# Optimization experiments

Hardware: AMD Instinct MI355X
Metric: run time of the kernel (lower is better)

Reference implementation:

```python
import jax, jax.numpy as jnp
import numpy as np

B, S, H, NH = 4, 2048, 1024, 16
HD = H // NH
SCALE = 1.0 / np.sqrt(HD)
MASK_VAL = -1e9  # fp32 branch of the torch code


def setup_inputs() -> dict:
    key = jax.random.key(0)
    ks = jax.random.split(key, 6)
    s = 1.0 / np.sqrt(H)
    return {
        "x": jax.random.normal(ks[0], (B, S, H), dtype=jnp.float32),
        "attention_mask": jnp.ones((B, S), dtype=jnp.int32),
        "Wq": jax.random.normal(ks[1], (H, H), dtype=jnp.float32) * s,
        "Wk": jax.random.normal(ks[2], (H, H), dtype=jnp.float32) * s,
        "Wv": jax.random.normal(ks[3], (H, H), dtype=jnp.float32) * s,
        "Wo": jax.random.normal(ks[4], (H, H), dtype=jnp.float32) * s,
        "bo": jnp.zeros((H,), dtype=jnp.float32),
    }


def reference(x, attention_mask, Wq, Wk, Wv, Wo, bo):
    b, s, h = x.shape
    # projections; torch Linear computes x @ W.T
    q = (x @ Wq.T).reshape(b, s, NH, HD).transpose(0, 2, 1, 3)  # [b,nh,s,hd]
    k = (x @ Wk.T).reshape(b, s, NH, HD).transpose(0, 2, 1, 3)
    v = (x @ Wv.T).reshape(b, s, NH, HD).transpose(0, 2, 1, 3)

    scores = jnp.einsum("bhqd,bhkd->bhqk", q, k) * SCALE  # [b,nh,s,s]
    # padding mask: [b,1,1,s]
    pad = (attention_mask == 0)[:, None, None, :]
    scores = jnp.where(pad, MASK_VAL, scores)
    # causal mask
    causal = jnp.tril(jnp.ones((s, s), dtype=bool))[None, None]
    scores = jnp.where(causal, scores, MASK_VAL)

    attn = jax.nn.softmax(scores, axis=-1)  # dropout p=0 / eval -> identity
    out = jnp.einsum("bhqk,bhkd->bhqd", attn, v)
    out = out.transpose(0, 2, 1, 3).reshape(b, s, h)
    return out @ Wo.T + bo
```

## Files before the change

### kernel.cpp

```cpp
#include <hip/hip_runtime.h>

#define B_ 4
#define S_ 2048
#define H_ 1024
#define NH_ 16
#define HD_ 64
#define QSCALE_ 0.1803368801111204f

typedef __attribute__((ext_vector_type(8))) short bf16x8;
typedef __attribute__((ext_vector_type(4))) float f32x4;
typedef __attribute__((ext_vector_type(16))) float f32x16;

__device__ __forceinline__ unsigned short f2bf(float f) {
    unsigned u = __float_as_uint(f);
    unsigned r = (u + 0x7FFFu + ((u >> 16) & 1u)) >> 16;
    return (unsigned short)r;
}
__device__ __forceinline__ float exp2f_hw(float x) { return __builtin_amdgcn_exp2f(x); }

__global__ __launch_bounds__(256) void cast_all(const float* __restrict__ x,
                                                const float* __restrict__ Wq,
                                                const float* __restrict__ Wk,
                                                const float* __restrict__ Wv,
                                                const float* __restrict__ Wo,
                                                unsigned short* __restrict__ xb,
                                                unsigned short* __restrict__ Wqb,
                                                unsigned short* __restrict__ Wkb,
                                                unsigned short* __restrict__ Wvb,
                                                unsigned short* __restrict__ Wob) {
    int bid = blockIdx.x;
    const float* src;
    unsigned short* dst;
    int i;
    if (bid < 8192) {
        src = x; dst = xb; i = bid * 256 + threadIdx.x;
    } else {
        int k = bid - 8192, wsel = k >> 10;
        src = wsel == 0 ? Wq : wsel == 1 ? Wk : wsel == 2 ? Wv : Wo;
        dst = wsel == 0 ? Wqb : wsel == 1 ? Wkb : wsel == 2 ? Wvb : Wob;
        i = (k & 1023) * 256 + threadIdx.x;
    }
    float4 v = reinterpret_cast<const float4*>(src)[i];
    ushort4 o;
    o.x = f2bf(v.x); o.y = f2bf(v.y); o.z = f2bf(v.z); o.w = f2bf(v.w);
    reinterpret_cast<ushort4*>(dst)[i] = o;
}

__device__ __forceinline__ void stage128_swz(const char* g, int gstride, char* lds, int tid) {
    int wave = tid >> 6, lane = tid & 63;
#pragma unroll
    for (int j = 0; j < 4; ++j) {
        int o = ((wave * 4 + j) * 64 + lane) * 16;
        int r = o >> 7;
        int slot = (o >> 4) & 7;
        const char* src = g + (size_t)r * gstride + ((slot ^ (r & 7)) << 4);
        __builtin_amdgcn_global_load_lds((const __attribute__((address_space(1))) void*)src,
                                         (__attribute__((address_space(3))) void*)(lds + (wave * 4 + j) * 1024),
                                         16, 0, 0);
    }
}
__device__ __forceinline__ void stage64_swz8(const char* g, int gstride, char* lds, int tid) {
    int wave = tid >> 6, lane = tid & 63;
    int o = (wave * 64 + lane) * 16;
    int r = o >> 7;
    int slot = (o >> 4) & 7;
    const char* src = g + (size_t)r * gstride + ((slot ^ (r & 7)) << 4);
    __builtin_amdgcn_global_load_lds((const __attribute__((address_space(1))) void*)src,
                                     (__attribute__((address_space(3))) void*)(lds + wave * 1024 + lane * 16),
                                     16, 0, 0);
}

__device__ __forceinline__ bf16x8 frag_swz(const char* lds, int row, int slot) {
    return *reinterpret_cast<const bf16x8*>(lds + row * 128 + (((slot) ^ (row & 7)) << 4));
}

__device__ __forceinline__ float vmax16(const f32x16& v) {
    float a0 = fmaxf(v[0], v[1]), a1 = fmaxf(v[2], v[3]);
    float a2 = fmaxf(v[4], v[5]), a3 = fmaxf(v[6], v[7]);
    float a4 = fmaxf(v[8], v[9]), a5 = fmaxf(v[10], v[11]);
    float a6 = fmaxf(v[12], v[13]), a7 = fmaxf(v[14], v[15]);
    float b0 = fmaxf(a0, a1), b1 = fmaxf(a2, a3), b2 = fmaxf(a4, a5), b3 = fmaxf(a6, a7);
    return fmaxf(fmaxf(b0, b1), fmaxf(b2, b3));
}

__global__ __launch_bounds__(256) void gemm_qkv(const unsigned short* __restrict__ xb,
                                                const unsigned short* __restrict__ Wq,
                                                const unsigned short* __restrict__ Wk,
                                                const unsigned short* __restrict__ Wv,
                                                unsigned short* __restrict__ Qo,
                                                unsigned short* __restrict__ Ko,
                                                unsigned short* __restrict__ Vo) {
    __shared__ __align__(16) char As[2][16384];
    __shared__ __align__(16) char Bs[2][16384];
    int tid = threadIdx.x, lane = tid & 63, wave = tid >> 6;
    int wr = wave >> 1, wc = wave & 1;
    int brow = blockIdx.x * 128;
    int mat = blockIdx.y >> 3;
    int bcol = (blockIdx.y & 7) * 128;
    const unsigned short* W = mat == 0 ? Wq : (mat == 1 ? Wk : Wv);
    unsigned short* O = mat == 0 ? Qo : (mat == 1 ? Ko : Vo);
    float oscale = (mat == 0) ? QSCALE_ : 1.0f;
    f32x4 acc[4][4] = {};
    const char* ga = (const char*)(xb + (size_t)brow * H_);
    const char* gb = (const char*)(W + (size_t)bcol * H_);
    int ro = lane & 15, kg = lane >> 4;
    stage128_swz(ga, H_ * 2, As[0], tid);
    stage128_swz(gb, H_ * 2, Bs[0], tid);
    __syncthreads();
    for (int kt = 0; kt < 16; ++kt) {
        if (kt < 15) {
            stage128_swz(ga + (kt + 1) * 128, H_ * 2, As[(kt + 1) & 1], tid);
            stage128_swz(gb + (kt + 1) * 128, H_ * 2, Bs[(kt + 1) & 1], tid);
        }
        const char* Ac = As[kt & 1];
        const char* Bc = Bs[kt & 1];
#pragma unroll
        for (int kk = 0; kk < 2; ++kk) {
            bf16x8 af[4], bfr[4];
#pragma unroll
            for (int m = 0; m < 4; ++m) af[m] = frag_swz(Ac, wr * 64 + m * 16 + ro, kk * 4 + kg);
#pragma unroll
            for (int n = 0; n < 4; ++n) bfr[n] = frag_swz(Bc, wc * 64 + n * 16 + ro, kk * 4 + kg);
#pragma unroll
            for (int m = 0; m < 4; ++m)
#pragma unroll
                for (int n = 0; n < 4; ++n)
                    acc[m][n] = __builtin_amdgcn_mfma_f32_16x16x32_bf16(bfr[n], af[m], acc[m][n], 0, 0, 0);
        }
        __syncthreads();
    }
#pragma unroll
    for (int m = 0; m < 4; ++m) {
        int grow = brow + wr * 64 + m * 16 + ro;
#pragma unroll
        for (int n = 0; n < 4; ++n) {
            int gcol = bcol + wc * 64 + n * 16 + kg * 4;
            float p0 = acc[m][n][0] * oscale, p1 = acc[m][n][1] * oscale;
            float p2 = acc[m][n][2] * oscale, p3 = acc[m][n][3] * oscale;
            unsigned w0, w1;
            asm("v_cvt_pk_bf16_f32 %0, %1, %2" : "=v"(w0) : "v"(p0), "v"(p1));
            asm("v_cvt_pk_bf16_f32 %0, %1, %2" : "=v"(w1) : "v"(p2), "v"(p3));
            uint2 pk; pk.x = w0; pk.y = w1;
            *reinterpret_cast<uint2*>(O + (size_t)grow * H_ + gcol) = pk;
        }
    }
}

__global__ __launch_bounds__(256) void gemm_out(const unsigned short* __restrict__ Ab,
                                                const unsigned short* __restrict__ Wo,
                                                const float* __restrict__ bo,
                                                float* __restrict__ out) {
    __shared__ __align__(16) char As[2][16384];
    __shared__ __align__(16) char Bs[2][16384];
    int tid = threadIdx.x, lane = tid & 63, wave = tid >> 6;
    int wr = wave >> 1, wc = wave & 1;
    int brow = blockIdx.x * 128;
    int bcol = blockIdx.y * 128;
    f32x4 acc[4][4] = {};
    const char* ga = (const char*)(Ab + (size_t)brow * H_);
    const char* gb = (const char*)(Wo + (size_t)bcol * H_);
    int ro = lane & 15, kg = lane >> 4;
    stage128_swz(ga, H_ * 2, As[0], tid);
    stage128_swz(gb, H_ * 2, Bs[0], tid);
    __syncthreads();
    for (int kt = 0; kt < 16; ++kt) {
        if (kt < 15) {
            stage128_swz(ga + (kt + 1) * 128, H_ * 2, As[(kt + 1) & 1], tid);
            stage128_swz(gb + (kt + 1) * 128, H_ * 2, Bs[(kt + 1) & 1], tid);
        }
        const char* Ac = As[kt & 1];
        const char* Bc = Bs[kt & 1];
#pragma unroll
        for (int kk = 0; kk < 2; ++kk) {
            bf16x8 af[4], bfr[4];
#pragma unroll
            for (int m = 0; m < 4; ++m) af[m] = frag_swz(Ac, wr * 64 + m * 16 + ro, kk * 4 + kg);
#pragma unroll
            for (int n = 0; n < 4; ++n) bfr[n] = frag_swz(Bc, wc * 64 + n * 16 + ro, kk * 4 + kg);
#pragma unroll
            for (int m = 0; m < 4; ++m)
#pragma unroll
                for (int n = 0; n < 4; ++n)
                    acc[m][n] = __builtin_amdgcn_mfma_f32_16x16x32_bf16(bfr[n], af[m], acc[m][n], 0, 0, 0);
        }
        __syncthreads();
    }
#pragma unroll
    for (int m = 0; m < 4; ++m) {
        int grow = brow + wr * 64 + m * 16 + ro;
#pragma unroll
        for (int n = 0; n < 4; ++n) {
            int gcol = bcol + wc * 64 + n * 16 + kg * 4;
            float4 bn4 = *reinterpret_cast<const float4*>(bo + gcol);
            float4 o4;
            o4.x = acc[m][n][0] + bn4.x;
            o4.y = acc[m][n][1] + bn4.y;
            o4.z = acc[m][n][2] + bn4.z;
            o4.w = acc[m][n][3] + bn4.w;
            *reinterpret_cast<float4*>(out + (size_t)grow * H_ + gcol) = o4;
        }
    }
}

__global__ __launch_bounds__(512) void attn(const unsigned short* __restrict__ Q,
                                            const unsigned short* __restrict__ K,
                                            const unsigned short* __restrict__ V,
                                            const int* __restrict__ amask,
                                            unsigned short* __restrict__ Ab) {
    __shared__ __align__(16) char lds[32768];
    char* Ksm = lds;
    unsigned short* Vt = (unsigned short*)(lds + 16384);
    unsigned char* maskc = (unsigned char*)(lds + 24576);
    unsigned char* anyz = (unsigned char*)(lds + 26624);

    int tid = threadIdx.x, lane = tid & 63, w = tid >> 6;
    int l31 = lane & 31, hi = lane >> 5, hi4 = hi * 4;
    int id = blockIdx.x;
    int g = id >> 6;
    int qb = (g < 4) ? (7 - 2 * g) : (2 * g - 8);
    int bh = id & 63, b = bh >> 4, h = bh & 15;
    int brow = qb * 256;
    int Qwg = brow + w * 32;

    unsigned cm = 0;
#pragma unroll
    for (int r = 0; r < 16; ++r)
        if (((r & 3) + 8 * (r >> 2) + hi4) > l31) cm |= (1u << r);

    const unsigned short* Qg = Q + (size_t)(b * S_ + Qwg + l31) * H_ + h * HD_;
    const unsigned short* Kg = K + (size_t)b * S_ * H_ + h * HD_;
    const unsigned short* Vg = V + (size_t)b * S_ * H_ + h * HD_;

    stage64_swz8((const char*)Kg, H_ * 2, Ksm, tid);
    int vr = tid & 63, vd0 = (tid >> 6) * 8;
    bf16x8 vreg = *reinterpret_cast<const bf16x8*>(Vg + (size_t)vr * H_ + vd0);
    {
        const int4* am4 = reinterpret_cast<const int4*>(amask + b * S_);
        int i = tid;
        if (i < S_ / 4) {
            int4 v = am4[i];
            uchar4 o;
            o.x = (v.x == 0); o.y = (v.y == 0); o.z = (v.z == 0); o.w = (v.w == 0);
            reinterpret_cast<uchar4*>(maskc)[i] = o;
        }
    }
    bf16x8 qf[4];
#pragma unroll
    for (int kk = 0; kk < 4; ++kk)
        qf[kk] = *reinterpret_cast<const bf16x8*>(Qg + kk * 16 + hi * 8);

    __syncthreads();
    if (tid < 32) {
        const unsigned* mw = reinterpret_cast<const unsigned*>(maskc + tid * 64);
        unsigned o = 0;
#pragma unroll
        for (int i = 0; i < 16; ++i) o |= mw[i];
        anyz[tid] = o ? 1 : 0;
    }

    f32x16 oacc0, oacc1;
#pragma unroll
    for (int j = 0; j < 16; ++j) { oacc0[j] = 0.f; oacc1[j] = 0.f; }
    float mrun = -__builtin_inff(), lrun = 0.f;

    int T = 4 * qb + 4;
    for (int t = 0; t < T; ++t) {
        int kv0 = t * 64;
        const char* Kc = Ksm + (t & 1) * 8192;

        {
            unsigned short* vb = Vt + vd0 * 64 + (vr & 7);
            int rs3 = (vr >> 3) << 3;
#pragma unroll
            for (int j = 0; j < 8; ++j)
                vb[j * 64 + (rs3 ^ (j << 3))] = (unsigned short)vreg[j];
        }
        __syncthreads();

        if (t + 1 < T)
            stage64_swz8((const char*)(Kg + (size_t)(kv0 + 64) * H_), H_ * 2,
                         Ksm + ((t + 1) & 1) * 8192, tid);
        {
            int kvn = (t + 1 < T) ? kv0 + 64 : kv0;
            vreg = *reinterpret_cast<const bf16x8*>(Vg + (size_t)(kvn + vr) * H_ + vd0);
        }

        int c0 = kv0, c1 = kv0 + 32;
        if (c0 <= Qwg) {
            bool vis1 = (c1 <= Qwg);
            f32x16 sa0, sa1;
#pragma unroll
            for (int j = 0; j < 16; ++j) { sa0[j] = 0.f; sa1[j] = 0.f; }

            __builtin_amdgcn_s_setprio(1);
#pragma unroll
            for (int kk = 0; kk < 4; ++kk) {
                bf16x8 kf0 = frag_swz(Kc, l31, 2 * kk + hi);
                sa0 = __builtin_amdgcn_mfma_f32_32x32x16_bf16(kf0, qf[kk], sa0, 0, 0, 0);
                if (vis1) {
                    bf16x8 kf1 = frag_swz(Kc, 32 + l31, 2 * kk + hi);
                    sa1 = __builtin_amdgcn_mfma_f32_32x32x16_bf16(kf1, qf[kk], sa1, 0, 0, 0);
                }
            }
            __builtin_amdgcn_s_setprio(0);

            if (c0 == Qwg) {
#pragma unroll
                for (int r = 0; r < 16; ++r) sa0[r] = (cm & (1u << r)) ? -1e9f : sa0[r];
            }
            if (vis1 && c1 == Qwg) {
#pragma unroll
                for (int r = 0; r < 16; ++r) sa1[r] = (cm & (1u << r)) ? -1e9f : sa1[r];
            }
            if (anyz[t]) {
#pragma unroll
                for (int u = 0; u < 4; ++u) {
                    uchar4 mk = *reinterpret_cast<const uchar4*>(maskc + kv0 + 8 * u + hi4);
                    if (mk.x) sa0[4 * u + 0] = -1e9f;
                    if (mk.y) sa0[4 * u + 1] = -1e9f;
                    if (mk.z) sa0[4 * u + 2] = -1e9f;
                    if (mk.w) sa0[4 * u + 3] = -1e9f;
                }
                if (vis1) {
#pragma unroll
                    for (int u = 0; u < 4; ++u) {
                        uchar4 mk = *reinterpret_cast<const uchar4*>(maskc + kv0 + 32 + 8 * u + hi4);
                        if (mk.x) sa1[4 * u + 0] = -1e9f;
                        if (mk.y) sa1[4 * u + 1] = -1e9f;
                        if (mk.z) sa1[4 * u + 2] = -1e9f;
                        if (mk.w) sa1[4 * u + 3] = -1e9f;
                    }
                }
            }

            float mx = vmax16(sa0);
            if (vis1) mx = fmaxf(mx, vmax16(sa1));
            mx = fmaxf(mx, __shfl_xor(mx, 32));

            if (__any(mx > mrun + 10.f)) {
                float mnew = fmaxf(mrun, mx);
                float fsc = exp2f_hw(mrun - mnew);
                mrun = mnew;
                lrun *= fsc;
#pragma unroll
                for (int j = 0; j < 16; ++j) { oacc0[j] *= fsc; oacc1[j] *= fsc; }
            }

            float rs = 0.f;
            __builtin_amdgcn_s_setprio(1);
#pragma unroll
            for (int n = 0; n < 2; ++n) {
                if (n == 1 && !vis1) break;
                const f32x16& sa = (n == 0) ? sa0 : sa1;
                unsigned int wrd[4][2];
#pragma unroll
                for (int u = 0; u < 4; ++u) {
                    float p0 = exp2f_hw(sa[4 * u + 0] - mrun);
                    float p1 = exp2f_hw(sa[4 * u + 1] - mrun);
                    float p2 = exp2f_hw(sa[4 * u + 2] - mrun);
                    float p3 = exp2f_hw(sa[4 * u + 3] - mrun);
                    rs += (p0 + p1) + (p2 + p3);
                    asm("v_cvt_pk_bf16_f32 %0, %1, %2" : "=v"(wrd[u][0]) : "v"(p0), "v"(p1));
                    asm("v_cvt_pk_bf16_f32 %0, %1, %2" : "=v"(wrd[u][1]) : "v"(p2), "v"(p3));
                }
#pragma unroll
                for (int half = 0; half < 2; ++half) {
                    int u0 = 2 * half;
                    unsigned int X0 = wrd[u0][0], Y0 = wrd[u0 + 1][0];
                    unsigned int X1 = wrd[u0][1], Y1 = wrd[u0 + 1][1];
                    asm("v_permlane32_swap_b32 %0, %1" : "+v"(X0), "+v"(Y0));
                    asm("v_permlane32_swap_b32 %0, %1" : "+v"(X1), "+v"(Y1));
                    union { unsigned int u[4]; bf16x8 v; } bu;
                    bu.u[0] = X0; bu.u[1] = X1; bu.u[2] = Y0; bu.u[3] = Y1;
                    int kc = 2 * n + half;
                    bf16x8 af0 = *reinterpret_cast<const bf16x8*>(
                        &Vt[(l31) * 64 + (((2 * kc + hi) ^ (l31 & 7)) << 3)]);
                    oacc0 = __builtin_amdgcn_mfma_f32_32x32x16_bf16(af0, bu.v, oacc0, 0, 0, 0);
                    bf16x8 af1 = *reinterpret_cast<const bf16x8*>(
                        &Vt[(32 + l31) * 64 + (((2 * kc + hi) ^ (l31 & 7)) << 3)]);
                    oacc1 = __builtin_amdgcn_mfma_f32_32x32x16_bf16(af1, bu.v, oacc1, 0, 0, 0);
                }
            }
            __builtin_amdgcn_s_setprio(0);

            rs += __shfl_xor(rs, 32);
            lrun += rs;
        }
        __syncthreads();
    }

    float inv = 1.f / lrun;
    unsigned short* Osm = reinterpret_cast<unsigned short*>(lds);
#pragma unroll
    for (int r = 0; r < 16; ++r) {
        int d = (r & 3) + 8 * (r >> 2) + hi4;
        Osm[w * 2048 + l31 * 64 + ((((d >> 3) ^ (l31 & 7)) << 3) | (d & 7))] = f2bf(oacc0[r] * inv);
        int d1 = d + 32;
        Osm[w * 2048 + l31 * 64 + ((((d1 >> 3) ^ (l31 & 7)) << 3) | (d1 & 7))] = f2bf(oacc1[r] * inv);
    }
    __syncthreads();
#pragma unroll
    for (int wv = 0; wv < 4; ++wv) {
        int q = tid >> 3, j = tid & 7;
        int row = wv * 64 + q;
        bf16x8 vv = *reinterpret_cast<const bf16x8*>(
            Osm + (row >> 5) * 2048 + (row & 31) * 64 + ((j ^ (row & 7)) << 3));
        size_t grow = (size_t)(b * S_ + brow + row);
        *reinterpret_cast<bf16x8*>(Ab + grow * H_ + h * HD_ + j * 8) = vv;
    }
}

extern "C" void kernel_launch(void* const* d_in, const int* in_sizes, int n_in,
                              void* d_out, int out_size, void* d_ws, size_t ws_size,
                              hipStream_t stream) {
    const float* x  = (const float*)d_in[0];
    const int* amask = (const int*)d_in[1];
    const float* Wq = (const float*)d_in[2];
    const float* Wk = (const float*)d_in[3];
    const float* Wv = (const float*)d_in[4];
    const float* Wo = (const float*)d_in[5];
    const float* bo = (const float*)d_in[6];
    float* out = (float*)d_out;

    const size_t XN = (size_t)B_ * S_ * H_;
    const size_t WN = (size_t)H_ * H_;

    char* ws = (char*)d_ws;
    unsigned short* xb  = (unsigned short*)ws;           ws += XN * 2;
    unsigned short* Wqb = (unsigned short*)ws;           ws += WN * 2;
    unsigned short* Wkb = (unsigned short*)ws;           ws += WN * 2;
    unsigned short* Wvb = (unsigned short*)ws;           ws += WN * 2;
    unsigned short* Wob = (unsigned short*)ws;           ws += WN * 2;
    unsigned short* Qb  = (unsigned short*)ws;           ws += XN * 2;
    unsigned short* Kb  = (unsigned short*)ws;           ws += XN * 2;
    unsigned short* Vb  = (unsigned short*)ws;           ws += XN * 2;
    unsigned short* Ab  = (unsigned short*)ws;           ws += XN * 2;

    cast_all<<<12288, 256, 0, stream>>>(x, Wq, Wk, Wv, Wo, xb, Wqb, Wkb, Wvb, Wob);
    gemm_qkv<<<dim3(64, 24), 256, 0, stream>>>(xb, Wqb, Wkb, Wvb, Qb, Kb, Vb);
    attn<<<512, 512, 0, stream>>>(Qb, Kb, Vb, amask, Ab);
    gemm_out<<<dim3(64, 8), 256, 0, stream>>>(Ab, Wob, bo, out);
}
```

Before: 172.0 us.

## Single-buffer GEMM LDS and remap attention blocks across XCDs for head locality

The QKV and output GEMMs go from double-buffered LDS staging to a single buffer: each k-step loads a tile, syncs and computes. This halves LDS per block (64KB to 32KB) so more blocks can be resident per CU, at the cost of losing load/compute overlap and adding a sync per iteration. The attention kernel's block-to-work mapping is changed so that blocks landing on the same XCD (blockIdx mod 8) share batch-head pairs, improving L2 reuse of K/V. It also mirrors the causal query-block order for half of the heads to balance load.

```diff
diff --git a/kernel.cpp b/kernel.cpp
--- a/kernel.cpp
+++ b/kernel.cpp
@@ -90,8 +90,8 @@
                                                 unsigned short* __restrict__ Qo,
                                                 unsigned short* __restrict__ Ko,
                                                 unsigned short* __restrict__ Vo) {
-    __shared__ __align__(16) char As[2][16384];
-    __shared__ __align__(16) char Bs[2][16384];
+    __shared__ __align__(16) char As[16384];
+    __shared__ __align__(16) char Bs[16384];
     int tid = threadIdx.x, lane = tid & 63, wave = tid >> 6;
     int wr = wave >> 1, wc = wave & 1;
     int brow = blockIdx.x * 128;
@@ -104,23 +104,17 @@
     const char* ga = (const char*)(xb + (size_t)brow * H_);
     const char* gb = (const char*)(W + (size_t)bcol * H_);
     int ro = lane & 15, kg = lane >> 4;
-    stage128_swz(ga, H_ * 2, As[0], tid);
-    stage128_swz(gb, H_ * 2, Bs[0], tid);
-    __syncthreads();
     for (int kt = 0; kt < 16; ++kt) {
-        if (kt < 15) {
-            stage128_swz(ga + (kt + 1) * 128, H_ * 2, As[(kt + 1) & 1], tid);
-            stage128_swz(gb + (kt + 1) * 128, H_ * 2, Bs[(kt + 1) & 1], tid);
-        }
-        const char* Ac = As[kt & 1];
-        const char* Bc = Bs[kt & 1];
+        stage128_swz(ga + kt * 128, H_ * 2, As, tid);
+        stage128_swz(gb + kt * 128, H_ * 2, Bs, tid);
+        __syncthreads();
 #pragma unroll
         for (int kk = 0; kk < 2; ++kk) {
             bf16x8 af[4], bfr[4];
 #pragma unroll
-            for (int m = 0; m < 4; ++m) af[m] = frag_swz(Ac, wr * 64 + m * 16 + ro, kk * 4 + kg);
-#pragma unroll
-            for (int n = 0; n < 4; ++n) bfr[n] = frag_swz(Bc, wc * 64 + n * 16 + ro, kk * 4 + kg);
+            for (int m = 0; m < 4; ++m) af[m] = frag_swz(As, wr * 64 + m * 16 + ro, kk * 4 + kg);
+#pragma unroll
+            for (int n = 0; n < 4; ++n) bfr[n] = frag_swz(Bs, wc * 64 + n * 16 + ro, kk * 4 + kg);
 #pragma unroll
             for (int m = 0; m < 4; ++m)
 #pragma unroll
@@ -150,8 +144,8 @@
                                                 const unsigned short* __restrict__ Wo,
                                                 const float* __restrict__ bo,
                                                 float* __restrict__ out) {
-    __shared__ __align__(16) char As[2][16384];
-    __shared__ __align__(16) char Bs[2][16384];
+    __shared__ __align__(16) char As[16384];
+    __shared__ __align__(16) char Bs[16384];
     int tid = threadIdx.x, lane = tid & 63, wave = tid >> 6;
     int wr = wave >> 1, wc = wave & 1;
     int brow = blockIdx.x * 128;
@@ -160,23 +154,17 @@
     const char* ga = (const char*)(Ab + (size_t)brow * H_);
     const char* gb = (const char*)(Wo + (size_t)bcol * H_);
     int ro = lane & 15, kg = lane >> 4;
-    stage128_swz(ga, H_ * 2, As[0], tid);
-    stage128_swz(gb, H_ * 2, Bs[0], tid);
-    __syncthreads();
     for (int kt = 0; kt < 16; ++kt) {
-        if (kt < 15) {
-            stage128_swz(ga + (kt + 1) * 128, H_ * 2, As[(kt + 1) & 1], tid);
-            stage128_swz(gb + (kt + 1) * 128, H_ * 2, Bs[(kt + 1) & 1], tid);
-        }
-        const char* Ac = As[kt & 1];
-        const char* Bc = Bs[kt & 1];
+        stage128_swz(ga + kt * 128, H_ * 2, As, tid);
+        stage128_swz(gb + kt * 128, H_ * 2, Bs, tid);
+        __syncthreads();
 #pragma unroll
         for (int kk = 0; kk < 2; ++kk) {
             bf16x8 af[4], bfr[4];
 #pragma unroll
-            for (int m = 0; m < 4; ++m) af[m] = frag_swz(Ac, wr * 64 + m * 16 + ro, kk * 4 + kg);
-#pragma unroll
-            for (int n = 0; n < 4; ++n) bfr[n] = frag_swz(Bc, wc * 64 + n * 16 + ro, kk * 4 + kg);
+            for (int m = 0; m < 4; ++m) af[m] = frag_swz(As, wr * 64 + m * 16 + ro, kk * 4 + kg);
+#pragma unroll
+            for (int n = 0; n < 4; ++n) bfr[n] = frag_swz(Bs, wc * 64 + n * 16 + ro, kk * 4 + kg);
 #pragma unroll
             for (int m = 0; m < 4; ++m)
 #pragma unroll
@@ -215,10 +203,15 @@
 
     int tid = threadIdx.x, lane = tid & 63, w = tid >> 6;
     int l31 = lane & 31, hi = lane >> 5, hi4 = hi * 4;
-    int id = blockIdx.x;
-    int g = id >> 6;
-    int qb = (g < 4) ? (7 - 2 * g) : (2 * g - 8);
-    int bh = id & 63, b = bh >> 4, h = bh & 15;
+    int i = blockIdx.x;
+    int xcd = i & 7;
+    int slot = i >> 3;
+    int bh_hi = slot >> 3;
+    int qsel = slot & 7;
+    int bh = bh_hi * 8 + xcd;
+    int b = bh >> 4, h = bh & 15;
+    int qbt = (qsel < 4) ? (7 - 2 * qsel) : (2 * qsel - 8);
+    int qb = (bh_hi < 4) ? qbt : 7 - qbt;
     int brow = qb * 256;
     int Qwg = brow + w * 32;
 
@@ -236,12 +229,12 @@
     bf16x8 vreg = *reinterpret_cast<const bf16x8*>(Vg + (size_t)vr * H_ + vd0);
     {
         const int4* am4 = reinterpret_cast<const int4*>(amask + b * S_);
-        int i = tid;
-        if (i < S_ / 4) {
-            int4 v = am4[i];
+        int ii = tid;
+        if (ii < S_ / 4) {
+            int4 v = am4[ii];
             uchar4 o;
             o.x = (v.x == 0); o.y = (v.y == 0); o.z = (v.z == 0); o.w = (v.w == 0);
-            reinterpret_cast<uchar4*>(maskc)[i] = o;
+            reinterpret_cast<uchar4*>(maskc)[ii] = o;
         }
     }
     bf16x8 qf[4];
@@ -254,7 +247,7 @@
         const unsigned* mw = reinterpret_cast<const unsigned*>(maskc + tid * 64);
         unsigned o = 0;
 #pragma unroll
-        for (int i = 0; i < 16; ++i) o |= mw[i];
+        for (int ii = 0; ii < 16; ++ii) o |= mw[ii];
         anyz[tid] = o ? 1 : 0;
     }
 
```

Result: no change. 172.7 us (+0.4%).
